# Optimization experiments

Measured on AMD Instinct MI355X. Metric: run time of the kernel, lower is better.

## Reference

```python
import jax, jax.numpy as jnp
import numpy as np

A = 256          # image height (x_shape[0])
B = 256          # image width  (x_shape[1])
N = 64           # filterbank grid size
H_DIM = 1024     # hidden dim
BATCH = 512
MAX_DIM = max(A, B)


def _compute_F(params):
    """Build NxA and NxB Gaussian filterbank matrices from 5 attention params.
    Faithful to the torch code: .item() calls on g_X, g_Y, d cut gradients,
    replicated here with stop_gradient; global (not row-wise) normalization;
    var = exp(params[2] + 1e-8) as in the source."""
    gt_X, gt_Y = params[0], params[1]
    var = jnp.exp(params[2] + 1e-8)
    dt = jnp.exp(params[3])
    g_X = jax.lax.stop_gradient((A + 1) * (gt_X + 1) / 2)
    g_Y = jax.lax.stop_gradient((B + 1) * (gt_Y + 1) / 2)
    d = jax.lax.stop_gradient(dt * (MAX_DIM - 1) / (N - 1))
    sub_val = (-N * 0.5 - 0.5) * d  # first linspace endpoint offset; step == d
    idx = jnp.arange(N, dtype=params.dtype)
    mu_X = g_X + sub_val + d * idx  # == linspace(g_X+sub, g_X+add, N)
    mu_Y = g_Y + sub_val + d * idx
    a = jnp.arange(A, dtype=params.dtype)
    b = jnp.arange(B, dtype=params.dtype)
    F_X = jnp.exp(-(a[None, :] - mu_X[:, None]) ** 2 / (2 * var))  # [N, A]
    F_Y = jnp.exp(-(b[None, :] - mu_Y[:, None]) ** 2 / (2 * var))  # [N, B]
    F_X = F_X / jnp.sum(F_X)
    F_Y = F_Y / jnp.sum(F_Y)
    return F_X, F_Y


def setup_inputs() -> dict:
    key = jax.random.key(0)
    k1, k2, k3, k4, k5 = jax.random.split(key, 5)
    x = jax.random.uniform(k1, (BATCH, A * B), dtype=jnp.float32)
    x_hat = jax.random.normal(k2, (BATCH, A * B), dtype=jnp.float32)
    h = jax.random.normal(k3, (BATCH, H_DIM), dtype=jnp.float32)
    # small init scale keeps exp(params) in a sane range
    W_read_w = jax.random.normal(k4, (5, H_DIM), dtype=jnp.float32) * 0.02
    W_read_b = jax.random.normal(k5, (5,), dtype=jnp.float32) * 0.01
    return {"x": x, "x_hat": x_hat, "h": h, "W_read_w": W_read_w, "W_read_b": W_read_b}


def reference(x, x_hat, h, W_read_w, W_read_b):
    # params from the FIRST batch element only, as in the torch code ([0])
    params = (h @ W_read_w.T + W_read_b)[0]  # [5]
    gamma = jnp.exp(params[4])
    F_X, F_Y = _compute_F(params)
    xi = x.reshape(-1, A, B)
    xh = x_hat.reshape(-1, A, B)

    def filt(im):
        # gamma * F_Y @ im @ F_X^T : [x, N, N]
        return gamma * jnp.einsum('na,xab,mb->xnm', F_Y, im, F_X)

    x_filt = filt(xi).reshape(-1, N * N)
    x_hat_filt = filt(xh).reshape(-1, N * N)
    return jnp.concatenate([x_filt, x_hat_filt], axis=1)  # [batch, 2*N^2]
```

## Files before the change

### kernel.cpp

```cpp
#include <hip/hip_runtime.h>
#include <math.h>

#define N_FILT 64
#define IMG_DIM 256
#define IMG_SZ (256*256)
#define HDIM 1024
#define NBATCH 512

typedef __attribute__((ext_vector_type(4))) float f32x4;
typedef __attribute__((address_space(3))) float lds_float;


__device__ __forceinline__ void gl_lds16(const float* g, float* l){
  __builtin_amdgcn_global_load_lds(
      (const __attribute__((address_space(1))) unsigned int*)g,
      (__attribute__((address_space(3))) unsigned int*)l,
      16, 0, 0);
}

__global__ __launch_bounds__(1024) void k_prep(
    const float* __restrict__ h, const float* __restrict__ Ww,
    const float* __restrict__ Wb, int* __restrict__ meta,
    float* __restrict__ fyg, float* __restrict__ fxg)
{
  __shared__ float partial[16*8];
  __shared__ float par_s[8];
  __shared__ float F[N_FILT*IMG_DIM];
  __shared__ int s_lo[64], s_hi[64], s_glo[16], s_ghi[16];
  __shared__ float ssum[16];
  const int t   = threadIdx.x;
  const int side= blockIdx.x;
  const int wv  = t>>6, ln = t&63;
  float* __restrict__ wout = side ? fxg : fyg;

  {
    float4 z = make_float4(0.f,0.f,0.f,0.f);
    float4* p = (float4*)wout;
    #pragma unroll
    for (int k=0;k<4;++k) p[t + 1024*k] = z;
  }

  {
    const float hv = h[t];
    float s0 = hv*Ww[t];
    float s1 = hv*Ww[HDIM+t];
    float s2 = hv*Ww[2*HDIM+t];
    float s3 = hv*Ww[3*HDIM+t];
    float s4 = hv*Ww[4*HDIM+t];
    #pragma unroll
    for (int o=32;o>0;o>>=1){
      s0+=__shfl_down(s0,o); s1+=__shfl_down(s1,o); s2+=__shfl_down(s2,o);
      s3+=__shfl_down(s3,o); s4+=__shfl_down(s4,o);
    }
    if (ln==0){ partial[wv*8+0]=s0; partial[wv*8+1]=s1; partial[wv*8+2]=s2;
                partial[wv*8+3]=s3; partial[wv*8+4]=s4; }
  }
  __syncthreads();
  if (t<5){
    float s = Wb[t];
    #pragma unroll
    for (int k=0;k<16;++k) s += partial[k*8+t];
    par_s[t] = s;
  }
  __syncthreads();

  const float var   = expf(par_s[2]+1e-8f);
  const float dt    = expf(par_s[3]);
  const float gamma = expf(par_s[4]);
  const float gC = 0.5f*257.f*(par_s[side?0:1]+1.f);
  const float d  = dt*(255.f/63.f);
  const float sub= -32.5f*d;
  const float inv2v = 1.f/(2.f*var);
  const float w88v  = 88.f*var;

  if (t<64){
    float mu = gC + sub + d*(float)t;
    float astar = fminf(255.f, fmaxf(0.f, rintf(mu)));
    float t0 = (astar-mu)*(astar-mu);
    float r  = sqrtf(t0 + w88v);
    int lo = (int)ceilf(mu-r); int hi = (int)floorf(mu+r)+1;
    lo = lo<0?0:lo; hi = hi>256?256:hi; if (hi<lo) hi=lo;
    s_lo[t]=lo; s_hi[t]=hi;
  }
  __syncthreads();
  if (t<16){
    int lo=256, hi=0;
    #pragma unroll
    for (int k2=0;k2<4;++k2){ lo=min(lo,s_lo[t*4+k2]); hi=max(hi,s_hi[t*4+k2]); }
    if (hi<lo){lo=0;hi=0;}
    if (side==0){ meta[t]=lo; meta[16+t]=hi; }
    else        { lo &= ~3;  meta[32+t]=lo; meta[48+t]=hi; }
    s_glo[t]=lo; s_ghi[t]=hi;
  }
  float sum=0.f;
  #pragma unroll
  for (int k=0;k<16;++k){
    int idx=t+1024*k;
    int n=idx>>8, a=idx&255;
    float mu = gC+sub+d*(float)n;
    float dx=(float)a-mu;
    float e=expf(-dx*dx*inv2v);
    F[idx]=e; sum+=e;
  }
  #pragma unroll
  for (int o=32;o>0;o>>=1) sum+=__shfl_down(sum,o);
  if (ln==0) ssum[wv]=sum;
  __syncthreads();
  float stot = 0.f;
  #pragma unroll
  for (int k=0;k<16;++k) stot += ssum[k];
  const float sc = (side==0 ? gamma : 1.f)/stot;
  #pragma unroll
  for (int k=0;k<16;++k){
    int idx=t+1024*k;
    int n=idx>>8, a=idx&255, g=n>>2;
    int lo=s_glo[g], hi=s_ghi[g];
    if (a>=lo && a<hi) wout[(size_t)((g<<10)+((a-lo)<<2)+(n&3))] = F[idx]*sc;
  }
}

__global__ __launch_bounds__(256, 2) void k_main(
    const float* __restrict__ x, const float* __restrict__ xh,
    const int* __restrict__ meta, const float* __restrict__ fyg,
    const float* __restrict__ fxg, float* __restrict__ out)
{
  __shared__ float POOL[16384];
  const int bid = blockIdx.x;
  const int lg  = ((bid&7)<<8) | (bid>>3);
  const int p   = lg>>2, qq = lg&3;
  const int tid = threadIdx.x;
  const int w    = __builtin_amdgcn_readfirstlane(tid>>6);
  const int lane = tid & 63;
  const float* __restrict__ srcA = x  + (size_t)p*IMG_SZ;
  const float* __restrict__ srcB = xh + (size_t)p*IMG_SZ;
  float* __restrict__ dstA = out + (size_t)p*8192 + qq*1024;
  float* __restrict__ dstB = dstA + 4096;

  float accA[4][4], accB[4][4];
  {
    const int g  = qq*4 + w;
    const int a0 = __builtin_amdgcn_readfirstlane(meta[g]);
    const int a1 = __builtin_amdgcn_readfirstlane(meta[16+g]);
    const int R  = a1 - a0;
    const int CC = (R + 1) >> 1;
    const float* const wp = fyg + ((size_t)g<<10);
    const float* const sA = srcA + (lane<<2);
    const float* const sB = srcB + (lane<<2);
    #pragma unroll
    for (int k2=0;k2<4;++k2){
      accA[k2][0]=0.f;accA[k2][1]=0.f;accA[k2][2]=0.f;accA[k2][3]=0.f;
      accB[k2][0]=0.f;accB[k2][1]=0.f;accB[k2][2]=0.f;accB[k2][3]=0.f;
    }

#define DMA4(ch) do{ const int _c=(ch); const int _r0=a0+2*_c; \
    float* const _b = &POOL[(w<<12) + ((_c&3)<<10)]; \
    gl_lds16(sA + ((size_t)min(_r0,  255)<<8), _b); \
    gl_lds16(sB + ((size_t)min(_r0,  255)<<8), _b+256); \
    gl_lds16(sA + ((size_t)min(_r0+1,255)<<8), _b+512); \
    gl_lds16(sB + ((size_t)min(_r0+1,255)<<8), _b+768); }while(0)
#define FMAROW(ACC,W,T) do{ \
    ACC[0][0]=fmaf(W.x,T.x,ACC[0][0]); ACC[0][1]=fmaf(W.x,T.y,ACC[0][1]); \
    ACC[0][2]=fmaf(W.x,T.z,ACC[0][2]); ACC[0][3]=fmaf(W.x,T.w,ACC[0][3]); \
    ACC[1][0]=fmaf(W.y,T.x,ACC[1][0]); ACC[1][1]=fmaf(W.y,T.y,ACC[1][1]); \
    ACC[1][2]=fmaf(W.y,T.z,ACC[1][2]); ACC[1][3]=fmaf(W.y,T.w,ACC[1][3]); \
    ACC[2][0]=fmaf(W.z,T.x,ACC[2][0]); ACC[2][1]=fmaf(W.z,T.y,ACC[2][1]); \
    ACC[2][2]=fmaf(W.z,T.z,ACC[2][2]); ACC[2][3]=fmaf(W.z,T.w,ACC[2][3]); \
    ACC[3][0]=fmaf(W.w,T.x,ACC[3][0]); ACC[3][1]=fmaf(W.w,T.y,ACC[3][1]); \
    ACC[3][2]=fmaf(W.w,T.z,ACC[3][2]); ACC[3][3]=fmaf(W.w,T.w,ACC[3][3]); }while(0)

    if (R > 0){
      DMA4(0); DMA4(1); DMA4(2);
      #pragma unroll 1
      for (int c=0; c<CC; ++c){
        DMA4(c+3);
        __builtin_amdgcn_sched_barrier(0);
        asm volatile("s_waitcnt vmcnt(12)");
        __builtin_amdgcn_sched_barrier(0);
        f32x4 tA0,tB0,tA1,tB1;
        lds_float* l0 = (lds_float*)&POOL[(w<<12) + ((c&3)<<10) + (lane<<2)];
        asm volatile("ds_read_b128 %0, %1"             : "=&v"(tA0) : "v"(l0));
        asm volatile("ds_read_b128 %0, %1 offset:1024" : "=&v"(tB0) : "v"(l0));
        asm volatile("ds_read_b128 %0, %1 offset:2048" : "=&v"(tA1) : "v"(l0));
        asm volatile("ds_read_b128 %0, %1 offset:3072" : "=&v"(tB1) : "v"(l0));
        const f32x4 w0 = ((const f32x4*)wp)[min(2*c,  255)];
        const f32x4 w1 = ((const f32x4*)wp)[min(2*c+1,255)];
        asm volatile("s_waitcnt lgkmcnt(0)");
        __builtin_amdgcn_sched_barrier(0);
        FMAROW(accA,w0,tA0); FMAROW(accB,w0,tB0);
        FMAROW(accA,w1,tA1); FMAROW(accB,w1,tB1);
      }
      asm volatile("s_waitcnt vmcnt(0)");
    }
#undef DMA4
  }
  __syncthreads();
  #pragma unroll
  for (int k2=0;k2<4;++k2){
    const int n = w*4 + k2;
    float4 va; va.x=accA[k2][0]; va.y=accA[k2][1]; va.z=accA[k2][2]; va.w=accA[k2][3];
    float4 vb; vb.x=accB[k2][0]; vb.y=accB[k2][1]; vb.z=accB[k2][2]; vb.w=accB[k2][3];
    *(float4*)&POOL[       (n<<8) + ((lane ^ n)<<2)] = va;
    *(float4*)&POOL[4096 + (n<<8) + ((lane ^ n)<<2)] = vb;
  }
  __syncthreads();

  const int nl = lane & 15;
  const int cc = lane >> 4;
  const int q  = w*4 + cc;
  const int lo4 = meta[32+q];
  const int hi  = meta[48+q];
  int ngu = (hi - lo4 + 3) >> 2;
  ngu = max(ngu, __shfl_xor(ngu,16));
  ngu = max(ngu, __shfl_xor(ngu,32));
  const int u0  = lo4 >> 2;
  const float* wq = fxg + ((size_t)q<<10);
  float oA0=0.f,oA1=0.f,oA2=0.f,oA3=0.f;
  float oB0=0.f,oB1=0.f,oB2=0.f,oB3=0.f;
  #pragma unroll 2
  for (int it=0; it<ngu; it+=2){
    const int uA_ = min(u0+it,   63);
    const int uB_ = min(u0+it+1, 63);
    const float4 tA0 = *(const float4*)&POOL[       (nl<<8) + ((uA_^nl)<<2)];
    const float4 tA1 = *(const float4*)&POOL[       (nl<<8) + ((uB_^nl)<<2)];
    const float4 tB0 = *(const float4*)&POOL[4096 + (nl<<8) + ((uA_^nl)<<2)];
    const float4 tB1 = *(const float4*)&POOL[4096 + (nl<<8) + ((uB_^nl)<<2)];
    const float4 a0w = *(const float4*)(wq + it*16);
    const float4 a1w = *(const float4*)(wq + it*16 + 4);
    const float4 a2w = *(const float4*)(wq + it*16 + 8);
    const float4 a3w = *(const float4*)(wq + it*16 + 12);
    const float4 b0w = *(const float4*)(wq + it*16 + 16);
    const float4 b1w = *(const float4*)(wq + it*16 + 20);
    const float4 b2w = *(const float4*)(wq + it*16 + 24);
    const float4 b3w = *(const float4*)(wq + it*16 + 28);
    oA0=fmaf(tA0.x,a0w.x,fmaf(tA0.y,a1w.x,fmaf(tA0.z,a2w.x,fmaf(tA0.w,a3w.x,oA0))));
    oA1=fmaf(tA0.x,a0w.y,fmaf(tA0.y,a1w.y,fmaf(tA0.z,a2w.y,fmaf(tA0.w,a3w.y,oA1))));
    oA2=fmaf(tA0.x,a0w.z,fmaf(tA0.y,a1w.z,fmaf(tA0.z,a2w.z,fmaf(tA0.w,a3w.z,oA2))));
    oA3=fmaf(tA0.x,a0w.w,fmaf(tA0.y,a1w.w,fmaf(tA0.z,a2w.w,fmaf(tA0.w,a3w.w,oA3))));
    oB0=fmaf(tB0.x,a0w.x,fmaf(tB0.y,a1w.x,fmaf(tB0.z,a2w.x,fmaf(tB0.w,a3w.x,oB0))));
    oB1=fmaf(tB0.x,a0w.y,fmaf(tB0.y,a1w.y,fmaf(tB0.z,a2w.y,fmaf(tB0.w,a3w.y,oB1))));
    oB2=fmaf(tB0.x,a0w.z,fmaf(tB0.y,a1w.z,fmaf(tB0.z,a2w.z,fmaf(tB0.w,a3w.z,oB2))));
    oB3=fmaf(tB0.x,a0w.w,fmaf(tB0.y,a1w.w,fmaf(tB0.z,a2w.w,fmaf(tB0.w,a3w.w,oB3))));
    if (it+1 < ngu){
      oA0=fmaf(tA1.x,b0w.x,fmaf(tA1.y,b1w.x,fmaf(tA1.z,b2w.x,fmaf(tA1.w,b3w.x,oA0))));
      oA1=fmaf(tA1.x,b0w.y,fmaf(tA1.y,b1w.y,fmaf(tA1.z,b2w.y,fmaf(tA1.w,b3w.y,oA1))));
      oA2=fmaf(tA1.x,b0w.z,fmaf(tA1.y,b1w.z,fmaf(tA1.z,b2w.z,fmaf(tA1.w,b3w.z,oA2))));
      oA3=fmaf(tA1.x,b0w.w,fmaf(tA1.y,b1w.w,fmaf(tA1.z,b2w.w,fmaf(tA1.w,b3w.w,oA3))));
      oB0=fmaf(tB1.x,b0w.x,fmaf(tB1.y,b1w.x,fmaf(tB1.z,b2w.x,fmaf(tB1.w,b3w.x,oB0))));
      oB1=fmaf(tB1.x,b0w.y,fmaf(tB1.y,b1w.y,fmaf(tB1.z,b2w.y,fmaf(tB1.w,b3w.y,oB1))));
      oB2=fmaf(tB1.x,b0w.z,fmaf(tB1.y,b1w.z,fmaf(tB1.z,b2w.z,fmaf(tB1.w,b3w.z,oB2))));
      oB3=fmaf(tB1.x,b0w.w,fmaf(tB1.y,b1w.w,fmaf(tB1.z,b2w.w,fmaf(tB1.w,b3w.w,oB3))));
    }
  }
  {
    const int m0 = q*4;
    POOL[8192 + nl*68 + m0 + 0] = oA0; POOL[8192 + nl*68 + m0 + 1] = oA1;
    POOL[8192 + nl*68 + m0 + 2] = oA2; POOL[8192 + nl*68 + m0 + 3] = oA3;
    POOL[9472 + nl*68 + m0 + 0] = oB0; POOL[9472 + nl*68 + m0 + 1] = oB1;
    POOL[9472 + nl*68 + m0 + 2] = oB2; POOL[9472 + nl*68 + m0 + 3] = oB3;
  }
  __syncthreads();
  {
    const int f = tid*4;
    const int n = f>>6, m = f&63;
    *(float4*)(dstA+f) = *(const float4*)&POOL[8192 + n*68 + m];
    *(float4*)(dstB+f) = *(const float4*)&POOL[9472 + n*68 + m];
  }
#undef FMAROW
}

extern "C" void kernel_launch(void* const* d_in, const int* in_sizes, int n_in,
                              void* d_out, int out_size, void* d_ws, size_t ws_size,
                              hipStream_t stream)
{
  const float* x  = (const float*)d_in[0];
  const float* xh = (const float*)d_in[1];
  const float* h  = (const float*)d_in[2];
  const float* Ww = (const float*)d_in[3];
  const float* Wb = (const float*)d_in[4];
  float* out = (float*)d_out;

  int*   meta = (int*)d_ws;
  float* fyg  = (float*)((char*)d_ws + 256);
  float* fxg  = (float*)((char*)d_ws + 256 + 65536);

  k_prep<<<2, 1024, 0, stream>>>(h, Ww, Wb, meta, fyg, fxg);
  k_main<<<4*NBATCH, 256, 0, stream>>>(x, xh, meta, fyg, fxg, out);
}
```

Measured before the change: 85.38 us.

## Replace LDS DMA pipeline with direct global loads and raise occupancy

Removes the global_load_lds four-stage ring buffer used in the row-reduction stage and replaces it with plain float4 global loads straight into registers in a simple unrolled loop. This halves the shared memory pool and raises launch bounds to 5 blocks per CU, relying on more resident waves rather than explicit software pipelining to hide memory latency. A barrier is added before the output staging so the reused LDS region is not overwritten while other waves still read it. The trade-off is losing explicit prefetch depth and asynchronous copies in exchange for occupancy, with possible register pressure under the tighter bound.

Measured after the change: 86.17 us. About the same (+0.9%).

```diff
diff --git a/kernel.cpp b/kernel.cpp
--- a/kernel.cpp
+++ b/kernel.cpp
@@ -8,15 +8,7 @@
 #define NBATCH 512
 
 typedef __attribute__((ext_vector_type(4))) float f32x4;
-typedef __attribute__((address_space(3))) float lds_float;
-
-
-__device__ __forceinline__ void gl_lds16(const float* g, float* l){
-  __builtin_amdgcn_global_load_lds(
-      (const __attribute__((address_space(1))) unsigned int*)g,
-      (__attribute__((address_space(3))) unsigned int*)l,
-      16, 0, 0);
-}
+
 
 __global__ __launch_bounds__(1024) void k_prep(
     const float* __restrict__ h, const float* __restrict__ Ww,
@@ -119,12 +111,12 @@
   }
 }
 
-__global__ __launch_bounds__(256, 2) void k_main(
+__global__ __launch_bounds__(256, 5) void k_main(
     const float* __restrict__ x, const float* __restrict__ xh,
     const int* __restrict__ meta, const float* __restrict__ fyg,
     const float* __restrict__ fxg, float* __restrict__ out)
 {
-  __shared__ float POOL[16384];
+  __shared__ float POOL[8192];
   const int bid = blockIdx.x;
   const int lg  = ((bid&7)<<8) | (bid>>3);
   const int p   = lg>>2, qq = lg&3;
@@ -142,22 +134,15 @@
     const int a0 = __builtin_amdgcn_readfirstlane(meta[g]);
     const int a1 = __builtin_amdgcn_readfirstlane(meta[16+g]);
     const int R  = a1 - a0;
-    const int CC = (R + 1) >> 1;
     const float* const wp = fyg + ((size_t)g<<10);
-    const float* const sA = srcA + (lane<<2);
-    const float* const sB = srcB + (lane<<2);
+    const float* const sA = srcA + ((size_t)a0<<8) + (lane<<2);
+    const float* const sB = srcB + ((size_t)a0<<8) + (lane<<2);
     #pragma unroll
     for (int k2=0;k2<4;++k2){
       accA[k2][0]=0.f;accA[k2][1]=0.f;accA[k2][2]=0.f;accA[k2][3]=0.f;
       accB[k2][0]=0.f;accB[k2][1]=0.f;accB[k2][2]=0.f;accB[k2][3]=0.f;
     }
 
-#define DMA4(ch) do{ const int _c=(ch); const int _r0=a0+2*_c; \
-    float* const _b = &POOL[(w<<12) + ((_c&3)<<10)]; \
-    gl_lds16(sA + ((size_t)min(_r0,  255)<<8), _b); \
-    gl_lds16(sB + ((size_t)min(_r0,  255)<<8), _b+256); \
-    gl_lds16(sA + ((size_t)min(_r0+1,255)<<8), _b+512); \
-    gl_lds16(sB + ((size_t)min(_r0+1,255)<<8), _b+768); }while(0)
 #define FMAROW(ACC,W,T) do{ \
     ACC[0][0]=fmaf(W.x,T.x,ACC[0][0]); ACC[0][1]=fmaf(W.x,T.y,ACC[0][1]); \
     ACC[0][2]=fmaf(W.x,T.z,ACC[0][2]); ACC[0][3]=fmaf(W.x,T.w,ACC[0][3]); \
@@ -168,30 +153,14 @@
     ACC[3][0]=fmaf(W.w,T.x,ACC[3][0]); ACC[3][1]=fmaf(W.w,T.y,ACC[3][1]); \
     ACC[3][2]=fmaf(W.w,T.z,ACC[3][2]); ACC[3][3]=fmaf(W.w,T.w,ACC[3][3]); }while(0)
 
-    if (R > 0){
-      DMA4(0); DMA4(1); DMA4(2);
-      #pragma unroll 1
-      for (int c=0; c<CC; ++c){
-        DMA4(c+3);
-        __builtin_amdgcn_sched_barrier(0);
-        asm volatile("s_waitcnt vmcnt(12)");
-        __builtin_amdgcn_sched_barrier(0);
-        f32x4 tA0,tB0,tA1,tB1;
-        lds_float* l0 = (lds_float*)&POOL[(w<<12) + ((c&3)<<10) + (lane<<2)];
-        asm volatile("ds_read_b128 %0, %1"             : "=&v"(tA0) : "v"(l0));
-        asm volatile("ds_read_b128 %0, %1 offset:1024" : "=&v"(tB0) : "v"(l0));
-        asm volatile("ds_read_b128 %0, %1 offset:2048" : "=&v"(tA1) : "v"(l0));
-        asm volatile("ds_read_b128 %0, %1 offset:3072" : "=&v"(tB1) : "v"(l0));
-        const f32x4 w0 = ((const f32x4*)wp)[min(2*c,  255)];
-        const f32x4 w1 = ((const f32x4*)wp)[min(2*c+1,255)];
-        asm volatile("s_waitcnt lgkmcnt(0)");
-        __builtin_amdgcn_sched_barrier(0);
-        FMAROW(accA,w0,tA0); FMAROW(accB,w0,tB0);
-        FMAROW(accA,w1,tA1); FMAROW(accB,w1,tB1);
-      }
-      asm volatile("s_waitcnt vmcnt(0)");
-    }
-#undef DMA4
+    #pragma unroll 2
+    for (int r=0; r<R; ++r){
+      const float4 tA = *(const float4* __restrict__)(sA + (r<<8));
+      const float4 tB = *(const float4* __restrict__)(sB + (r<<8));
+      const f32x4 wv = ((const f32x4*)wp)[r];
+      FMAROW(accA, wv, tA);
+      FMAROW(accB, wv, tB);
+    }
   }
   __syncthreads();
   #pragma unroll
@@ -251,19 +220,20 @@
       oB3=fmaf(tB1.x,b0w.w,fmaf(tB1.y,b1w.w,fmaf(tB1.z,b2w.w,fmaf(tB1.w,b3w.w,oB3))));
     }
   }
+  __syncthreads();
   {
     const int m0 = q*4;
-    POOL[8192 + nl*68 + m0 + 0] = oA0; POOL[8192 + nl*68 + m0 + 1] = oA1;
-    POOL[8192 + nl*68 + m0 + 2] = oA2; POOL[8192 + nl*68 + m0 + 3] = oA3;
-    POOL[9472 + nl*68 + m0 + 0] = oB0; POOL[9472 + nl*68 + m0 + 1] = oB1;
-    POOL[9472 + nl*68 + m0 + 2] = oB2; POOL[9472 + nl*68 + m0 + 3] = oB3;
+    POOL[       nl*68 + m0 + 0] = oA0; POOL[       nl*68 + m0 + 1] = oA1;
+    POOL[       nl*68 + m0 + 2] = oA2; POOL[       nl*68 + m0 + 3] = oA3;
+    POOL[1280 + nl*68 + m0 + 0] = oB0; POOL[1280 + nl*68 + m0 + 1] = oB1;
+    POOL[1280 + nl*68 + m0 + 2] = oB2; POOL[1280 + nl*68 + m0 + 3] = oB3;
   }
   __syncthreads();
   {
     const int f = tid*4;
     const int n = f>>6, m = f&63;
-    *(float4*)(dstA+f) = *(const float4*)&POOL[8192 + n*68 + m];
-    *(float4*)(dstB+f) = *(const float4*)&POOL[9472 + n*68 + m];
+    *(float4*)(dstA+f) = *(const float4*)&POOL[       n*68 + m];
+    *(float4*)(dstB+f) = *(const float4*)&POOL[1280 + n*68 + m];
   }
 #undef FMAROW
 }
```
